# Performance work log

Measured on AMD Instinct MI355X. Metric: run time of the kernel, lower is better.

Reference implementation:

```python
import jax, jax.numpy as jnp
import numpy as np

N_EMBD = 768
N_HEAD = 12
HEAD_DIM = N_EMBD // N_HEAD


def setup_inputs() -> dict:
    key = jax.random.key(0)
    k1, k2, k3, k4, k5 = jax.random.split(key, 5)
    B, T, C = 8, 1024, N_EMBD
    s = 0.02
    return {
        "x": jax.random.normal(k1, (B, T, C), dtype=jnp.float32),
        "w_attn": jax.random.normal(k2, (C, 3 * C), dtype=jnp.float32) * s,
        "b_attn": jnp.zeros((3 * C,), dtype=jnp.float32),
        "w_proj": jax.random.normal(k3, (C, C), dtype=jnp.float32) * s,
        "b_proj": jnp.zeros((C,), dtype=jnp.float32),
    }


def reference(x, w_attn, b_attn, w_proj, b_proj):
    B, T, C = x.shape
    H, D = N_HEAD, HEAD_DIM
    qkv = x @ w_attn + b_attn                      # [B,T,3C]
    q, k, v = jnp.split(qkv, 3, axis=-1)
    # [B,H,T,D]
    q = q.reshape(B, T, H, D).transpose(0, 2, 1, 3)
    k = k.reshape(B, T, H, D).transpose(0, 2, 1, 3)
    v = v.reshape(B, T, H, D).transpose(0, 2, 1, 3)
    att = jnp.einsum("bhqd,bhkd->bhqk", q, k) / jnp.sqrt(jnp.float32(D))
    causal = jnp.tril(jnp.ones((T, T), dtype=bool))
    att = jnp.where(causal[None, None], att, jnp.float32(-jnp.inf))
    att = jax.nn.softmax(att, axis=-1)
    y = jnp.einsum("bhqk,bhkd->bhqd", att, v)      # [B,H,T,D]
    y = y.transpose(0, 2, 1, 3).reshape(B, T, C)
    return y @ w_proj + b_proj
```

## Files before the change

### kernel.cpp

```cpp
#include <hip/hip_runtime.h>
#include <hip/hip_bf16.h>
#include <math.h>
#include <type_traits>

#define BATCH 8
#define SEQ   1024
#define NEMBD 768
#define NHEAD 12
#define HDIM  64
#define TC    (3 * NEMBD)

typedef __attribute__((ext_vector_type(4))) float f32x4;
typedef __attribute__((ext_vector_type(8))) short s16x8;

__device__ __forceinline__ unsigned short f2bf(float f) {
    return __builtin_bit_cast(unsigned short, __float2bfloat16(f));
}

__device__ __forceinline__ void gload_lds16(const void* g, void* l) {
    __builtin_amdgcn_global_load_lds(
        (const __attribute__((address_space(1))) void*)g,
        (__attribute__((address_space(3))) void*)l, 16, 0, 0);
}

__global__ __launch_bounds__(256) void cast_bf16_kernel(
    const float* __restrict__ in, unsigned short* __restrict__ out, int n)
{
    const int i = (blockIdx.x * 256 + threadIdx.x) * 8;
    float4 a = *(const float4*)(in + i);
    float4 b = *(const float4*)(in + i + 4);
    s16x8 v;
    v[0] = f2bf(a.x); v[1] = f2bf(a.y); v[2] = f2bf(a.z); v[3] = f2bf(a.w);
    v[4] = f2bf(b.x); v[5] = f2bf(b.y); v[6] = f2bf(b.z); v[7] = f2bf(b.w);
    *(s16x8*)(out + i) = v;
}

__global__ __launch_bounds__(256) void transpose_cast_kernel(
    const float* __restrict__ w, unsigned short* __restrict__ wT, int K, int N)
{
    __shared__ float t[32][33];
    const int tx = threadIdx.x, ty = threadIdx.y;
    const int n0 = blockIdx.x * 32, k0 = blockIdx.y * 32;
    #pragma unroll
    for (int i = 0; i < 4; ++i)
        t[ty + i * 8][tx] = w[(size_t)(k0 + ty + i * 8) * N + n0 + tx];
    __syncthreads();
    #pragma unroll
    for (int i = 0; i < 4; ++i)
        wT[(size_t)(n0 + ty + i * 8) * K + k0 + tx] = f2bf(t[tx][ty + i * 8]);
}

__global__ __launch_bounds__(256) void gemm_proj_kernel(
    const unsigned short* __restrict__ A,
    const unsigned short* __restrict__ Bt,
    const float* __restrict__ bias,
    float* __restrict__ C,
    int M, int N, int K, int nbn)
{
    constexpr int BUF = 16384;
    __shared__ __align__(16) char SM[3 * BUF];

    const int tid  = threadIdx.x;
    const int w    = tid >> 6, lane = tid & 63;
    const int lr   = lane & 15, lg = lane >> 4;
    const int wr   = w >> 1, wc = w & 1;

    const int swz = (blockIdx.x & 7) * (gridDim.x >> 3) + (blockIdx.x >> 3);
    const int bm = (swz / nbn) * 128, bn = (swz % nbn) * 128;

    const int srow = tid >> 2;
    const int gcol = ((tid & 3) ^ ((srow >> 1) & 3)) * 8;
    const unsigned short* Ag = A  + (size_t)(bm + srow) * K + gcol;
    const unsigned short* Bg = Bt + (size_t)(bn + srow) * K + gcol;

    const int NT = K >> 5;

    f32x4 acc[4][4];
    #pragma unroll
    for (int m = 0; m < 4; ++m)
        #pragma unroll
        for (int n = 0; n < 4; ++n) acc[m][n] = (f32x4){0.f, 0.f, 0.f, 0.f};

    auto stage = [&](int t) {
        const int k0 = t << 5;
        char* buf = SM + (t % 3) * BUF;
        #pragma unroll
        for (int p = 0; p < 2; ++p)
            gload_lds16(Ag + (size_t)(p * 64) * K + k0, buf + p * 4096 + tid * 16);
        #pragma unroll
        for (int p = 0; p < 2; ++p)
            gload_lds16(Bg + (size_t)(p * 64) * K + k0,
                        buf + 8192 + p * 4096 + tid * 16);
    };

    stage(0);
    stage(1);
    asm volatile("s_waitcnt vmcnt(4)" ::: "memory");
    __builtin_amdgcn_sched_barrier(0);
    __builtin_amdgcn_s_barrier();
    __builtin_amdgcn_sched_barrier(0);

    for (int t = 0; t < NT; ++t) {
        const char* buf = SM + (t % 3) * BUF;
        const bool more = (t + 2 < NT);
        if (more) stage(t + 2);

        s16x8 af[4], bfr[4];
        #pragma unroll
        for (int m = 0; m < 4; ++m) {
            const int ar = wr * 64 + m * 16 + lr;
            af[m] = *(const s16x8*)(buf + ar * 64 + ((lg ^ ((ar >> 1) & 3)) * 16));
        }
        #pragma unroll
        for (int n = 0; n < 4; ++n) {
            const int br = wc * 64 + n * 16 + lr;
            bfr[n] = *(const s16x8*)(buf + 8192 + br * 64
                                         + ((lg ^ ((br >> 1) & 3)) * 16));
        }

        __builtin_amdgcn_s_setprio(1);
        #pragma unroll
        for (int m = 0; m < 4; ++m)
            #pragma unroll
            for (int n = 0; n < 4; ++n)
                acc[m][n] = __builtin_amdgcn_mfma_f32_16x16x32_bf16(
                    af[m], bfr[n], acc[m][n], 0, 0, 0);
        __builtin_amdgcn_s_setprio(0);

        if (more) asm volatile("s_waitcnt vmcnt(4)" ::: "memory");
        else      asm volatile("s_waitcnt vmcnt(0)" ::: "memory");
        __builtin_amdgcn_sched_barrier(0);
        __builtin_amdgcn_s_barrier();
        __builtin_amdgcn_sched_barrier(0);
    }

    #pragma unroll
    for (int n = 0; n < 4; ++n) {
        const int col = bn + wc * 64 + n * 16 + lr;
        const float bv = bias[col];
        #pragma unroll
        for (int m = 0; m < 4; ++m) {
            const int row0 = bm + wr * 64 + m * 16 + lg * 4;
            #pragma unroll
            for (int r = 0; r < 4; ++r)
                C[(size_t)(row0 + r) * N + col] = acc[m][n][r] + bv;
        }
    }
}

__global__ __launch_bounds__(512) void gemm_qkv256_kernel(
    const unsigned short* __restrict__ A,
    const unsigned short* __restrict__ Bt,
    const float* __restrict__ bias,
    unsigned short* __restrict__ Qb,
    unsigned short* __restrict__ Kb,
    unsigned short* __restrict__ Vtb,
    int M, int K, int nbn)
{
    constexpr int BUF = 24576;
    __shared__ __align__(16) char SM[3 * BUF];

    const int tid  = threadIdx.x;
    const int w    = tid >> 6, lane = tid & 63;
    const int lr   = lane & 15, lg = lane >> 4;
    const int wr   = w >> 1, wc = w & 1;

    const int swz = (blockIdx.x & 7) * (gridDim.x >> 3) + (blockIdx.x >> 3);
    const int bm = (swz / nbn) * 256, bn = (swz % nbn) * 128;

    const int srow = tid >> 2;
    const int gcol = ((tid & 3) ^ ((srow >> 1) & 3)) * 8;
    const unsigned short* Ag = A  + (size_t)(bm + srow) * K + gcol;
    const unsigned short* Bg = Bt + (size_t)(bn + srow) * K + gcol;

    const int NT = K >> 5;

    f32x4 acc[4][4];
    #pragma unroll
    for (int m = 0; m < 4; ++m)
        #pragma unroll
        for (int n = 0; n < 4; ++n) acc[m][n] = (f32x4){0.f, 0.f, 0.f, 0.f};

    auto stage = [&](int t) {
        const int k0 = t << 5;
        char* buf = SM + (t % 3) * BUF;
        gload_lds16(Ag + k0,                   buf + tid * 16);
        gload_lds16(Ag + (size_t)128 * K + k0, buf + 8192 + tid * 16);
        gload_lds16(Bg + k0,                   buf + 16384 + tid * 16);
    };

    stage(0);
    stage(1);
    asm volatile("s_waitcnt vmcnt(3)" ::: "memory");
    __builtin_amdgcn_sched_barrier(0);
    __builtin_amdgcn_s_barrier();
    __builtin_amdgcn_sched_barrier(0);

    for (int t = 0; t < NT; ++t) {
        const char* buf = SM + (t % 3) * BUF;
        const bool more = (t + 2 < NT);
        if (more) stage(t + 2);

        s16x8 af[4], bfr[4];
        #pragma unroll
        for (int m = 0; m < 4; ++m) {
            const int ar = wr * 64 + m * 16 + lr;
            af[m] = *(const s16x8*)(buf + ar * 64 + ((lg ^ ((ar >> 1) & 3)) * 16));
        }
        #pragma unroll
        for (int n = 0; n < 4; ++n) {
            const int br = wc * 64 + n * 16 + lr;
            bfr[n] = *(const s16x8*)(buf + 16384 + br * 64
                                         + ((lg ^ ((br >> 1) & 3)) * 16));
        }

        __builtin_amdgcn_s_setprio(1);
        #pragma unroll
        for (int m = 0; m < 4; ++m)
            #pragma unroll
            for (int n = 0; n < 4; ++n)
                acc[m][n] = __builtin_amdgcn_mfma_f32_16x16x32_bf16(
                    af[m], bfr[n], acc[m][n], 0, 0, 0);
        __builtin_amdgcn_s_setprio(0);

        if (more) asm volatile("s_waitcnt vmcnt(3)" ::: "memory");
        else      asm volatile("s_waitcnt vmcnt(0)" ::: "memory");
        __builtin_amdgcn_sched_barrier(0);
        __builtin_amdgcn_s_barrier();
        __builtin_amdgcn_sched_barrier(0);
    }

    char* Ep = SM + w * 8192;

    const int region = bn / NEMBD;
    const int hh = ((bn % NEMBD) >> 6) + wc;
    const int row0 = bm + wr * 64;
    const int bb = row0 >> 10, t0 = row0 & 1023;
    const float scl = (region == 0) ? 0.1803368801111354f : 1.0f;

    float bvn[4];
    #pragma unroll
    for (int n = 0; n < 4; ++n) bvn[n] = bias[bn + wc * 64 + n * 16 + lr];

    if (region == 2) {
        #pragma unroll
        for (int m = 0; m < 4; ++m)
            #pragma unroll
            for (int n = 0; n < 4; ++n) {
                ushort4 pk;
                pk.x = f2bf(acc[m][n][0] + bvn[n]);
                pk.y = f2bf(acc[m][n][1] + bvn[n]);
                pk.z = f2bf(acc[m][n][2] + bvn[n]);
                pk.w = f2bf(acc[m][n][3] + bvn[n]);
                const int row = n * 16 + lr;
                const int lc  = m * 2 + (lg >> 1);
                *(ushort4*)(Ep + row * 128 + ((lc ^ (lr & 7)) * 16)
                               + (lg & 1) * 8) = pk;
            }
    } else {
        #pragma unroll
        for (int m = 0; m < 4; ++m)
            #pragma unroll
            for (int n = 0; n < 4; ++n)
                #pragma unroll
                for (int r = 0; r < 4; ++r) {
                    const int row = m * 16 + lg * 4 + r;
                    const int lc  = n * 2 + (lr >> 3);
                    *(unsigned short*)(Ep + row * 128
                        + ((lc ^ (row & 7)) * 16) + (lr & 7) * 2) =
                        f2bf((acc[m][n][r] + bvn[n]) * scl);
                }
    }
    asm volatile("s_waitcnt lgkmcnt(0)" ::: "memory");
    __builtin_amdgcn_sched_barrier(0);

    const int rr0 = lane >> 3;
    const int cc  = lane & 7;
    if (region == 2) {
        unsigned short* dst = Vtb + (((size_t)bb * NHEAD + hh) * HDIM) * SEQ + t0;
        #pragma unroll
        for (int it = 0; it < 8; ++it) {
            const int d = it * 8 + rr0;
            s16x8 v = *(const s16x8*)(Ep + d * 128 + ((cc ^ (d & 7)) * 16));
            *(s16x8*)(dst + (size_t)d * SEQ + cc * 8) = v;
        }
    } else {
        unsigned short* dst = (region == 0 ? Qb : Kb)
                            + ((size_t)bb * NHEAD + hh) * SEQ * HDIM;
        #pragma unroll
        for (int it = 0; it < 8; ++it) {
            const int t = it * 8 + rr0;
            s16x8 v = *(const s16x8*)(Ep + t * 128 + ((cc ^ (t & 7)) * 16));
            *(s16x8*)(dst + (size_t)(t0 + t) * HDIM + cc * 8) = v;
        }
    }
}

__global__ __launch_bounds__(256) void attn_mfma_kernel(
    const unsigned short* __restrict__ Qb,
    const unsigned short* __restrict__ Kb,
    const unsigned short* __restrict__ Vtb,
    unsigned short* __restrict__ y)
{
    const int bid  = blockIdx.x;
    const int xcd  = bid & 7;
    const int grp  = bid >> 3;
    const int pair = grp & 7;
    const int bh   = xcd + 8 * (grp >> 3);
    const int b    = bh / NHEAD, h = bh % NHEAD;

    const int tid  = threadIdx.x;
    const int w    = tid >> 6;
    const int lane = tid & 63;
    const int lr   = lane & 15;
    const int lg   = lane >> 4;

    __shared__ __align__(16) unsigned short Ks[64 * 72];
    __shared__ __align__(16) unsigned short Vs[64 * 72];
    __shared__ __align__(16) unsigned short Ps[4][16][72];

    const unsigned short* Kg = Kb  + (size_t)bh * SEQ * HDIM;
    const unsigned short* Vg = Vtb + (size_t)bh * HDIM * SEQ;

    const int sr = tid >> 2;
    const int sc = (tid & 3) * 16;
    const unsigned short* Kgr = Kg + (size_t)sr * HDIM + sc;
    const unsigned short* Vgr = Vg + (size_t)sr * SEQ  + sc;
    unsigned short* KsW = Ks + sr * 72 + sc;
    unsigned short* VsW = Vs + sr * 72 + sc;

    auto process = [&](int qt) {
        const unsigned short* Qg =
            Qb + ((size_t)bh * SEQ + qt * 64 + w * 16) * HDIM;
        s16x8 qf[2];
        #pragma unroll
        for (int kc = 0; kc < 2; ++kc)
            qf[kc] = *(const s16x8*)(Qg + (size_t)lr * HDIM + kc * 32 + lg * 8);

        f32x4 acc[4];
        #pragma unroll
        for (int df = 0; df < 4; ++df) acc[df] = (f32x4){0.f, 0.f, 0.f, 0.f};
        float lrow = 0.f;

        const int NT   = qt + 1;
        const int qrow = qt * 64 + w * 16 + lr;

        s16x8 krA = *(const s16x8*)(Kgr);
        s16x8 krB = *(const s16x8*)(Kgr + 8);
        s16x8 vrA = *(const s16x8*)(Vgr);
        s16x8 vrB = *(const s16x8*)(Vgr + 8);

        for (int kt = 0; kt < NT; ++kt) {
            __syncthreads();
            *(s16x8*)(KsW)     = krA;
            *(s16x8*)(KsW + 8) = krB;
            *(s16x8*)(VsW)     = vrA;
            *(s16x8*)(VsW + 8) = vrB;
            __syncthreads();
            if (kt + 1 < NT) {
                krA = *(const s16x8*)(Kgr + (size_t)(kt + 1) * 64 * HDIM);
                krB = *(const s16x8*)(Kgr + (size_t)(kt + 1) * 64 * HDIM + 8);
                vrA = *(const s16x8*)(Vgr + (kt + 1) * 64);
                vrB = *(const s16x8*)(Vgr + (kt + 1) * 64 + 8);
            }

            f32x4 sf[4];
            __builtin_amdgcn_s_setprio(1);
            #pragma unroll
            for (int s = 0; s < 4; ++s) {
                const unsigned short* kr = &Ks[(s * 16 + lr) * 72 + lg * 8];
                s16x8 a0 = *(const s16x8*)(kr);
                s16x8 a1 = *(const s16x8*)(kr + 32);
                sf[s] = __builtin_amdgcn_mfma_f32_16x16x32_bf16(
                    a0, qf[0], (f32x4){0.f, 0.f, 0.f, 0.f}, 0, 0, 0);
                sf[s] = __builtin_amdgcn_mfma_f32_16x16x32_bf16(a1, qf[1], sf[s], 0, 0, 0);
            }
            __builtin_amdgcn_s_setprio(0);

            float sv[4][4];
            #pragma unroll
            for (int s = 0; s < 4; ++s)
                #pragma unroll
                for (int r = 0; r < 4; ++r)
                    sv[s][r] = sf[s][r];
            if (kt == NT - 1) {
                const int kbase = kt * 64;
                #pragma unroll
                for (int s = 0; s < 4; ++s)
                    #pragma unroll
                    for (int r = 0; r < 4; ++r)
                        if (kbase + s * 16 + lg * 4 + r > qrow)
                            sv[s][r] = -INFINITY;
            }

            #pragma unroll
            for (int s = 0; s < 4; ++s) {
                float p0 = exp2f(sv[s][0]);
                float p1 = exp2f(sv[s][1]);
                float p2 = exp2f(sv[s][2]);
                float p3 = exp2f(sv[s][3]);
                lrow += (p0 + p1) + (p2 + p3);
                ushort4 pk;
                pk.x = f2bf(p0); pk.y = f2bf(p1); pk.z = f2bf(p2); pk.w = f2bf(p3);
                *(ushort4*)&Ps[w][lr][s * 16 + lg * 4] = pk;
            }

            asm volatile("s_waitcnt lgkmcnt(0)" ::: "memory");
            __builtin_amdgcn_sched_barrier(0);
            s16x8 pa[2];
            #pragma unroll
            for (int kc = 0; kc < 2; ++kc)
                pa[kc] = *(const s16x8*)&Ps[w][lr][kc * 32 + lg * 8];

            __builtin_amdgcn_s_setprio(1);
            #pragma unroll
            for (int df = 0; df < 4; ++df) {
                const unsigned short* vr = &Vs[(df * 16 + lr) * 72 + lg * 8];
                s16x8 va0 = *(const s16x8*)(vr);
                s16x8 va1 = *(const s16x8*)(vr + 32);
                acc[df] = __builtin_amdgcn_mfma_f32_16x16x32_bf16(va0, pa[0], acc[df], 0, 0, 0);
                acc[df] = __builtin_amdgcn_mfma_f32_16x16x32_bf16(va1, pa[1], acc[df], 0, 0, 0);
            }
            __builtin_amdgcn_s_setprio(0);
        }

        lrow += __shfl_xor(lrow, 16, 64);
        lrow += __shfl_xor(lrow, 32, 64);
        const float inv = 1.f / lrow;
        const int t = qt * 64 + w * 16 + lr;
        unsigned short* yp = y + ((size_t)(b * SEQ) + t) * NEMBD + h * HDIM;
        #pragma unroll
        for (int df = 0; df < 4; ++df) {
            ushort4 pk;
            pk.x = f2bf(acc[df][0] * inv);
            pk.y = f2bf(acc[df][1] * inv);
            pk.z = f2bf(acc[df][2] * inv);
            pk.w = f2bf(acc[df][3] * inv);
            *(ushort4*)(yp + df * 16 + lg * 4) = pk;
        }
    };

    process(15 - pair);
    process(pair);
}

extern "C" void kernel_launch(void* const* d_in, const int* in_sizes, int n_in,
                              void* d_out, int out_size, void* d_ws, size_t ws_size,
                              hipStream_t stream)
{
    const float* x      = (const float*)d_in[0];
    const float* w_attn = (const float*)d_in[1];
    const float* b_attn = (const float*)d_in[2];
    const float* w_proj = (const float*)d_in[3];
    const float* b_proj = (const float*)d_in[4];
    float* out = (float*)d_out;

    const int M = BATCH * SEQ;
    const size_t NQKV = (size_t)M * NEMBD;

    unsigned short* xb  = (unsigned short*)d_ws;
    unsigned short* waT = xb  + NQKV;
    unsigned short* wpT = waT + (size_t)TC * NEMBD;
    unsigned short* Qb  = wpT + (size_t)NEMBD * NEMBD;
    unsigned short* Kb  = Qb  + NQKV;
    unsigned short* Vtb = Kb  + NQKV;
    unsigned short* yb  = Vtb + NQKV;

    cast_bf16_kernel<<<(M * NEMBD) / 2048, 256, 0, stream>>>(x, xb, M * NEMBD);
    transpose_cast_kernel<<<dim3(TC / 32, NEMBD / 32), dim3(32, 8), 0, stream>>>(
        w_attn, waT, NEMBD, TC);
    transpose_cast_kernel<<<dim3(NEMBD / 32, NEMBD / 32), dim3(32, 8), 0, stream>>>(
        w_proj, wpT, NEMBD, NEMBD);

    gemm_qkv256_kernel<<<(M / 256) * (TC / 128), 512, 0, stream>>>(
        xb, waT, b_attn, Qb, Kb, Vtb, M, NEMBD, TC / 128);

    attn_mfma_kernel<<<768, 256, 0, stream>>>(Qb, Kb, Vtb, yb);

    gemm_proj_kernel<<<(NEMBD / 128) * (M / 128), 256, 0, stream>>>(
        yb, wpT, b_proj, out, M, NEMBD, NEMBD, NEMBD / 128);
}
```

Measured before the change: 106.8 us.

## Merge prep kernels into one launch and use 256x128 tiles for projection GEMM

The three preprocessing launches (input cast plus two weight transpose-casts) are folded into one kernel that picks its job from the block index, saving launch overhead. The output projection GEMM moves from 128x128 tiles with 256 threads to 256x128 tiles with 512 threads, so each B tile is reused across twice as many rows. The per-stage LDS buffer grows to 24KB and the waitcnt values change to match three loads per stage. The larger tile halves the grid, which may leave compute units underused on this small problem.

```diff
diff --git a/kernel.cpp b/kernel.cpp
--- a/kernel.cpp
+++ b/kernel.cpp
@@ -23,24 +23,36 @@
         (__attribute__((address_space(3))) void*)l, 16, 0, 0);
 }
 
-__global__ __launch_bounds__(256) void cast_bf16_kernel(
-    const float* __restrict__ in, unsigned short* __restrict__ out, int n)
+__global__ __launch_bounds__(256) void prep_kernel(
+    const float* __restrict__ x,
+    const float* __restrict__ w_attn,
+    const float* __restrict__ w_proj,
+    unsigned short* __restrict__ xb,
+    unsigned short* __restrict__ waT,
+    unsigned short* __restrict__ wpT)
 {
-    const int i = (blockIdx.x * 256 + threadIdx.x) * 8;
-    float4 a = *(const float4*)(in + i);
-    float4 b = *(const float4*)(in + i + 4);
-    s16x8 v;
-    v[0] = f2bf(a.x); v[1] = f2bf(a.y); v[2] = f2bf(a.z); v[3] = f2bf(a.w);
-    v[4] = f2bf(b.x); v[5] = f2bf(b.y); v[6] = f2bf(b.z); v[7] = f2bf(b.w);
-    *(s16x8*)(out + i) = v;
-}
-
-__global__ __launch_bounds__(256) void transpose_cast_kernel(
-    const float* __restrict__ w, unsigned short* __restrict__ wT, int K, int N)
-{
+    const int bid = blockIdx.x, tid = threadIdx.x;
+    if (bid < 3072) {
+        const int i = (bid * 256 + tid) * 8;
+        float4 a = *(const float4*)(x + i);
+        float4 b = *(const float4*)(x + i + 4);
+        s16x8 v;
+        v[0] = f2bf(a.x); v[1] = f2bf(a.y); v[2] = f2bf(a.z); v[3] = f2bf(a.w);
+        v[4] = f2bf(b.x); v[5] = f2bf(b.y); v[6] = f2bf(b.z); v[7] = f2bf(b.w);
+        *(s16x8*)(xb + i) = v;
+        return;
+    }
     __shared__ float t[32][33];
-    const int tx = threadIdx.x, ty = threadIdx.y;
-    const int n0 = blockIdx.x * 32, k0 = blockIdx.y * 32;
+    const float* w; unsigned short* wT; int K, N, bx, by;
+    if (bid < 4800) {
+        const int r = bid - 3072;
+        bx = r % 72; by = r / 72; w = w_attn; wT = waT; K = NEMBD; N = TC;
+    } else {
+        const int r = bid - 4800;
+        bx = r % 24; by = r / 24; w = w_proj; wT = wpT; K = NEMBD; N = NEMBD;
+    }
+    const int tx = tid & 31, ty = tid >> 5;
+    const int n0 = bx * 32, k0 = by * 32;
     #pragma unroll
     for (int i = 0; i < 4; ++i)
         t[ty + i * 8][tx] = w[(size_t)(k0 + ty + i * 8) * N + n0 + tx];
@@ -50,14 +62,14 @@
         wT[(size_t)(n0 + ty + i * 8) * K + k0 + tx] = f2bf(t[tx][ty + i * 8]);
 }
 
-__global__ __launch_bounds__(256) void gemm_proj_kernel(
+__global__ __launch_bounds__(512) void gemm_proj256_kernel(
     const unsigned short* __restrict__ A,
     const unsigned short* __restrict__ Bt,
     const float* __restrict__ bias,
     float* __restrict__ C,
     int M, int N, int K, int nbn)
 {
-    constexpr int BUF = 16384;
+    constexpr int BUF = 24576;
     __shared__ __align__(16) char SM[3 * BUF];
 
     const int tid  = threadIdx.x;
@@ -66,7 +78,7 @@
     const int wr   = w >> 1, wc = w & 1;
 
     const int swz = (blockIdx.x & 7) * (gridDim.x >> 3) + (blockIdx.x >> 3);
-    const int bm = (swz / nbn) * 128, bn = (swz % nbn) * 128;
+    const int bm = (swz / nbn) * 256, bn = (swz % nbn) * 128;
 
     const int srow = tid >> 2;
     const int gcol = ((tid & 3) ^ ((srow >> 1) & 3)) * 8;
@@ -84,18 +96,14 @@
     auto stage = [&](int t) {
         const int k0 = t << 5;
         char* buf = SM + (t % 3) * BUF;
-        #pragma unroll
-        for (int p = 0; p < 2; ++p)
-            gload_lds16(Ag + (size_t)(p * 64) * K + k0, buf + p * 4096 + tid * 16);
-        #pragma unroll
-        for (int p = 0; p < 2; ++p)
-            gload_lds16(Bg + (size_t)(p * 64) * K + k0,
-                        buf + 8192 + p * 4096 + tid * 16);
+        gload_lds16(Ag + k0,                   buf + tid * 16);
+        gload_lds16(Ag + (size_t)128 * K + k0, buf + 8192 + tid * 16);
+        gload_lds16(Bg + k0,                   buf + 16384 + tid * 16);
     };
 
     stage(0);
     stage(1);
-    asm volatile("s_waitcnt vmcnt(4)" ::: "memory");
+    asm volatile("s_waitcnt vmcnt(3)" ::: "memory");
     __builtin_amdgcn_sched_barrier(0);
     __builtin_amdgcn_s_barrier();
     __builtin_amdgcn_sched_barrier(0);
@@ -114,7 +122,7 @@
         #pragma unroll
         for (int n = 0; n < 4; ++n) {
             const int br = wc * 64 + n * 16 + lr;
-            bfr[n] = *(const s16x8*)(buf + 8192 + br * 64
+            bfr[n] = *(const s16x8*)(buf + 16384 + br * 64
                                          + ((lg ^ ((br >> 1) & 3)) * 16));
         }
 
@@ -127,7 +135,7 @@
                     af[m], bfr[n], acc[m][n], 0, 0, 0);
         __builtin_amdgcn_s_setprio(0);
 
-        if (more) asm volatile("s_waitcnt vmcnt(4)" ::: "memory");
+        if (more) asm volatile("s_waitcnt vmcnt(3)" ::: "memory");
         else      asm volatile("s_waitcnt vmcnt(0)" ::: "memory");
         __builtin_amdgcn_sched_barrier(0);
         __builtin_amdgcn_s_barrier();
@@ -466,17 +474,13 @@
     unsigned short* Vtb = Kb  + NQKV;
     unsigned short* yb  = Vtb + NQKV;
 
-    cast_bf16_kernel<<<(M * NEMBD) / 2048, 256, 0, stream>>>(x, xb, M * NEMBD);
-    transpose_cast_kernel<<<dim3(TC / 32, NEMBD / 32), dim3(32, 8), 0, stream>>>(
-        w_attn, waT, NEMBD, TC);
-    transpose_cast_kernel<<<dim3(NEMBD / 32, NEMBD / 32), dim3(32, 8), 0, stream>>>(
-        w_proj, wpT, NEMBD, NEMBD);
+    prep_kernel<<<5376, 256, 0, stream>>>(x, w_attn, w_proj, xb, waT, wpT);
 
     gemm_qkv256_kernel<<<(M / 256) * (TC / 128), 512, 0, stream>>>(
         xb, waT, b_attn, Qb, Kb, Vtb, M, NEMBD, TC / 128);
 
     attn_mfma_kernel<<<768, 256, 0, stream>>>(Qb, Kb, Vtb, yb);
 
-    gemm_proj_kernel<<<(NEMBD / 128) * (M / 128), 256, 0, stream>>>(
+    gemm_proj256_kernel<<<(M / 256) * (NEMBD / 128), 512, 0, stream>>>(
         yb, wpT, b_proj, out, M, NEMBD, NEMBD, NEMBD / 128);
 }
```

Result: faster. 103.1 us (-3.5%).
